# Kernel optimization log

Measured on AMD Instinct MI355X. Metric: run time of the kernel, lower is better.

The kernel has to match this reference:

```python
import jax, jax.numpy as jnp
import numpy as np

HSIZE, ESIZE, RSIZE = 256, 32, 64
STEP = 8  # dist=32, step=dist/4
B, A, T = 32, 128, 64

# 16 directional grid-cell bounds, shape [16,1,1] (matches torch constants)
_XMIN = jnp.array([STEP, 0, -STEP, -2 * STEP] * 4, jnp.float32).reshape(16, 1, 1)
_XMAX = jnp.array([2 * STEP, STEP, 0, -STEP] * 4, jnp.float32).reshape(16, 1, 1)
_YMIN = jnp.repeat(jnp.array([-2 * STEP, -STEP, 0, STEP], jnp.float32), 4).reshape(16, 1, 1)
_YMAX = jnp.repeat(jnp.array([-STEP, 0, STEP, 2 * STEP], jnp.float32), 4).reshape(16, 1, 1)


def setup_inputs() -> dict:
    key = jax.random.key(0)
    ks = jax.random.split(key, 20)
    w = lambda k, shape, s=0.05: jax.random.normal(k, shape, jnp.float32) * s
    data = jax.random.uniform(ks[0], (B, A, T, 2), jnp.float32) * 36.0 - 4.0
    return {
        "data": data,
        "tprob": 0,
        "W_r": w(ks[1], (RSIZE, 2)), "b_r": jnp.zeros((RSIZE,), jnp.float32),
        "W_e": w(ks[2], (ESIZE, HSIZE)), "b_e": jnp.zeros((ESIZE,), jnp.float32),
        "W_ih": w(ks[3], (4 * HSIZE, ESIZE * 16 + RSIZE)),
        "W_hh": w(ks[4], (4 * HSIZE, HSIZE)),
        "b_ih": jnp.zeros((4 * HSIZE,), jnp.float32),
        "b_hh": jnp.zeros((4 * HSIZE,), jnp.float32),
        "W_p": w(ks[5], (64, HSIZE + RSIZE)), "b_p": jnp.zeros((64,), jnp.float32),
        "W_p2": w(ks[6], (32, 64)), "b_p2": jnp.zeros((32,), jnp.float32),
        "W_mu": w(ks[7], (2, 32)), "b_mu": jnp.zeros((2,), jnp.float32),
        "W_sd": w(ks[8], (2, 32)), "b_sd": jnp.zeros((2,), jnp.float32),
        "W_cr": w(ks[9], (1, 32)), "b_cr": jnp.zeros((1,), jnp.float32),
    }


def _social(xy, h):
    # xy: [B,A,2] positions, h: [B,A,HSIZE] hidden states
    b, a = xy.shape[0], xy.shape[1]
    diff = xy[:, :, None, :] - xy[:, None, :, :]          # [B,A,A,2], (i,j)=x_i-x_j
    dx = diff[..., 0][:, None, :, :]                       # [B,1,A,A]
    dy = diff[..., 1][:, None, :, :]
    mask = (dx >= _XMIN) & (dx <= _XMAX) & (dy >= _YMIN) & (dy <= _YMAX)  # [B,16,A,A]
    active = xy[:, :, 0] >= 0                              # inactive: x<0
    mask = mask & active[:, None, :, None] & active[:, None, None, :]
    mask = mask & (~jnp.eye(a, dtype=bool))[None, None]    # zero diagonal
    # bmm: aggregate neighbor hiddens per grid cell
    return jnp.einsum('bgij,bjh->bgih', mask.astype(h.dtype), h)  # [B,16,A,HSIZE]


def reference(data, tprob, W_r, b_r, W_e, b_e, W_ih, W_hh, b_ih, b_hh,
              W_p, b_p, W_p2, b_p2, W_mu, b_mu, W_sd, b_sd, W_cr, b_cr):
    # tprob=0 -> teach_prob all zeros (no teacher forcing); dropout in eval mode.
    b, a, t, _ = data.shape
    h0 = jnp.zeros((b * a, HSIZE), data.dtype)
    c0 = jnp.zeros((b * a, HSIZE), data.dtype)

    def step(carry, xt):  # xt: [B,A,2]
        h, c = carry
        r = jax.nn.relu(xt @ W_r.T + b_r)                          # [B,A,64]
        Hs = _social(xt, h.reshape(b, a, HSIZE))                   # [B,16,A,256]
        e = jax.nn.relu(jnp.einsum('bgah,eh->bgae', Hs, W_e) + b_e)  # [B,16,A,32]
        e = e.reshape(b, a, 16 * ESIZE)                            # torch-style reshape
        inp = jnp.concatenate([r, e], -1).reshape(b * a, RSIZE + 16 * ESIZE)
        gates = inp @ W_ih.T + b_ih + h @ W_hh.T + b_hh
        ig, fg, gg, og = jnp.split(gates, 4, axis=-1)              # torch gate order i,f,g,o
        c2 = jax.nn.sigmoid(fg) * c + jax.nn.sigmoid(ig) * jnp.tanh(gg)
        h2 = jax.nn.sigmoid(og) * jnp.tanh(c2)
        inp2 = jnp.concatenate([r, h2.reshape(b, a, HSIZE)], -1)   # [B,A,320]
        out = (inp2 @ W_p.T + b_p) @ W_p2.T + b_p2                 # no activation (as in source)
        mu = out @ W_mu.T + b_mu
        sd = jnp.exp(out @ W_sd.T + b_sd)
        cr = jnp.tanh(out @ W_cr.T + b_cr)
        return (h2, c2), (mu, sd, cr)

    xs = jnp.moveaxis(data, 2, 0)                                  # [T,B,A,2]
    _, (mus, sds, crs) = jax.lax.scan(step, (h0, c0), xs)
    # stack along dim 2 -> [B,A,T,*]
    return (jnp.moveaxis(mus, 0, 2), jnp.moveaxis(sds, 0, 2), jnp.moveaxis(crs, 0, 2))
```

## Files before the change

### kernel.cpp

```cpp
#include <hip/hip_runtime.h>
#include <hip/hip_bf16.h>

#define B_  32
#define A_  128
#define T_  64
#define N_  4096
#define HS  256
#define ES  32
#define RS  64
#define KX  832
#define GD  1024
#define NKT 26

typedef __attribute__((ext_vector_type(8))) short bf8_t;
typedef __attribute__((ext_vector_type(8))) unsigned short u16x8;
typedef __attribute__((ext_vector_type(4))) float f4_t;
typedef __attribute__((ext_vector_type(2))) float f2_t;

__device__ __forceinline__ unsigned short f2bf(float x) {
  union { float f; unsigned u; } v; v.f = x;
  unsigned u = v.u;
  u += 0x7fffu + ((u >> 16) & 1u);
  return (unsigned short)(u >> 16);
}
__device__ __forceinline__ float bf2f(unsigned short u) {
  union { unsigned u; float f; } v; v.u = ((unsigned)u) << 16; return v.f;
}
__device__ __forceinline__ float sigm(float x) { return 1.f / (1.f + __expf(-x)); }

__device__ __forceinline__ void gload16(const void* g, void* l) {
  __builtin_amdgcn_global_load_lds((const __attribute__((address_space(1))) void*)g,
                                   (__attribute__((address_space(3))) void*)l, 16, 0, 0);
}

__global__ void k_wcat(const float* __restrict__ W_ih, const float* __restrict__ W_hh,
                       const float* __restrict__ b_ih, const float* __restrict__ b_hh,
                       const float* __restrict__ W_e,
                       unsigned short* __restrict__ Wc, float* __restrict__ bsum,
                       unsigned short* __restrict__ Web) {
  int i = blockIdx.x * 256 + threadIdx.x;
  if (i < GD * KX) {
    int mp = i / KX, k = i - mp * KX;
    int nb = mp >> 6, rem = mp & 63, g = rem >> 4, q = rem & 15;
    int mo = g * 256 + nb * 16 + q;
    float v = (k < 576) ? W_ih[mo * 576 + k] : W_hh[mo * 256 + (k - 576)];
    Wc[i] = f2bf(v);
  } else if (i < GD * KX + GD) {
    int j = i - GD * KX;
    int nb = j >> 6, rem = j & 63, g = rem >> 4, q = rem & 15;
    int mo = g * 256 + nb * 16 + q;
    bsum[j] = b_ih[mo] + b_hh[mo];
  } else if (i < GD * KX + GD + ES * HS) {
    int j2 = i - GD * KX - GD;
    Web[j2] = f2bf(W_e[j2]);
  }
}

__global__ __launch_bounds__(320) void k_head(
    const float* __restrict__ W_p, const float* __restrict__ b_p,
    const float* __restrict__ W_p2, const float* __restrict__ b_p2,
    const float* __restrict__ W_mu, const float* __restrict__ b_mu,
    const float* __restrict__ W_sd, const float* __restrict__ b_sd,
    const float* __restrict__ W_cr, const float* __restrict__ b_cr,
    float* __restrict__ Whead, float* __restrict__ bhead) {
  int o = blockIdx.x, tid = threadIdx.x;
  __shared__ float to[64];
  const float* Wo = (o < 2) ? W_mu + o * 32 : (o < 4) ? W_sd + (o - 2) * 32 : W_cr;
  if (tid < 64) {
    float a = 0.f;
    #pragma unroll 8
    for (int c = 0; c < 32; ++c) a += Wo[c] * W_p2[c * 64 + tid];
    to[tid] = a;
  }
  __syncthreads();
  float a = 0.f;
  #pragma unroll 8
  for (int j = 0; j < 64; ++j) a += to[j] * W_p[j * 320 + tid];
  Whead[o * 320 + tid] = a;
  if (tid == 0) {
    float b0 = (o < 2) ? b_mu[o] : (o < 4) ? b_sd[o - 2] : b_cr[0];
    float acc = b0;
    for (int c = 0; c < 32; ++c) acc += Wo[c] * b_p2[c];
    for (int j = 0; j < 64; ++j) acc += to[j] * b_p[j];
    bhead[o] = acc;
  }
}

__device__ __forceinline__ void head_fin_dev(
    const float* __restrict__ data, const float* __restrict__ W_r,
    const float* __restrict__ b_r, const float* __restrict__ Whead,
    const float* __restrict__ bhead, const unsigned short* __restrict__ Xh,
    float* __restrict__ out, int n0, int ts, int tid) {
  int r8 = tid >> 5, ln = tid & 31;
  int n = n0 + r8;
  float s0 = 0.f, s1 = 0.f, s2 = 0.f, s3 = 0.f, s4 = 0.f;
  u16x8 hv = *(const u16x8*)(Xh + (size_t)n * KX + 576 + ln * 8);
  float hf[8];
  #pragma unroll
  for (int k = 0; k < 8; ++k) hf[k] = bf2f(hv[k]);
  #pragma unroll
  for (int k = 0; k < 8; ++k) {
    int kk = 64 + ln * 8 + k;
    s0 += hf[k] * Whead[0 * 320 + kk];
    s1 += hf[k] * Whead[1 * 320 + kk];
    s2 += hf[k] * Whead[2 * 320 + kk];
    s3 += hf[k] * Whead[3 * 320 + kk];
    s4 += hf[k] * Whead[4 * 320 + kk];
  }
  float x0 = data[(n * T_ + ts) * 2 + 0];
  float x1 = data[(n * T_ + ts) * 2 + 1];
  #pragma unroll
  for (int l2 = 0; l2 < 2; ++l2) {
    int l = ln + 32 * l2;
    float rv = fmaxf(x0 * W_r[l * 2] + x1 * W_r[l * 2 + 1] + b_r[l], 0.f);
    s0 += rv * Whead[0 * 320 + l];
    s1 += rv * Whead[1 * 320 + l];
    s2 += rv * Whead[2 * 320 + l];
    s3 += rv * Whead[3 * 320 + l];
    s4 += rv * Whead[4 * 320 + l];
  }
  #pragma unroll
  for (int off = 16; off; off >>= 1) {
    s0 += __shfl_xor(s0, off);
    s1 += __shfl_xor(s1, off);
    s2 += __shfl_xor(s2, off);
    s3 += __shfl_xor(s3, off);
    s4 += __shfl_xor(s4, off);
  }
  if (ln == 0) {
    out[(n * T_ + ts) * 2 + 0] = s0 + bhead[0];
    out[(n * T_ + ts) * 2 + 1] = s1 + bhead[1];
    out[N_ * T_ * 2 + (n * T_ + ts) * 2 + 0] = __expf(s2 + bhead[2]);
    out[N_ * T_ * 2 + (n * T_ + ts) * 2 + 1] = __expf(s3 + bhead[3]);
    out[N_ * T_ * 4 + n * T_ + ts] = tanhf(s4 + bhead[4]);
  }
}

__global__ __launch_bounds__(256) void k_social(
    const float* __restrict__ data, const unsigned short* __restrict__ Web,
    const float* __restrict__ b_e, unsigned short* __restrict__ Xcur,
    const float* __restrict__ Whead, const float* __restrict__ bhead,
    const float* __restrict__ W_r, const float* __restrict__ b_r,
    float* __restrict__ out, int t) {
  int b  = blockIdx.x >> 4;
  int ig = blockIdx.x & 15;
  int n0 = b * A_ + ig * 8;
  __shared__ float sx[A_], sy[A_];
  __shared__ float shw2[64 * 64];
  __shared__ float smx[8][64][8];
  __shared__ float smy[8][64][8];
  int tid = threadIdx.x;
  if (tid < A_) {
    sx[tid] = data[((b * A_ + tid) * T_ + t) * 2 + 0];
    sy[tid] = data[((b * A_ + tid) * T_ + t) * 2 + 1];
  }
  if (t > 0)
    head_fin_dev(data, W_r, b_r, Whead, bhead, Xcur, out, n0, t - 1, tid);
  for (int u = tid; u < 512; u += 256) {
    int rr = u >> 6, l = u & 63;
    int n = n0 + rr;
    float x0 = data[(n * T_ + t) * 2 + 0];
    float x1 = data[(n * T_ + t) * 2 + 1];
    Xcur[(size_t)n * KX + l] =
        f2bf(fmaxf(x0 * W_r[l * 2] + x1 * W_r[l * 2 + 1] + b_r[l], 0.f));
  }
  {
    int wv = tid >> 6, lane = tid & 63;
    int lr = lane & 15, lh = lane >> 4;
    const unsigned short* a0p = Xcur + (size_t)(b * A_ + wv * 32 + lr) * KX + 576 + lh * 8;
    const unsigned short* a1p = a0p + 16 * KX;
    const unsigned short* b0p = Web + lr * HS + lh * 8;
    const unsigned short* b1p = Web + (16 + lr) * HS + lh * 8;
    f4_t hacc[2][2];
    hacc[0][0] = (f4_t){0.f,0.f,0.f,0.f}; hacc[0][1] = hacc[0][0];
    hacc[1][0] = hacc[0][0];              hacc[1][1] = hacc[0][0];
    #pragma unroll
    for (int kk = 0; kk < 8; ++kk) {
      bf8_t av0 = *(const bf8_t*)(a0p + kk * 32);
      bf8_t av1 = *(const bf8_t*)(a1p + kk * 32);
      bf8_t bv0 = *(const bf8_t*)(b0p + kk * 32);
      bf8_t bv1 = *(const bf8_t*)(b1p + kk * 32);
      hacc[0][0] = __builtin_amdgcn_mfma_f32_16x16x32_bf16(av0, bv0, hacc[0][0], 0, 0, 0);
      hacc[0][1] = __builtin_amdgcn_mfma_f32_16x16x32_bf16(av0, bv1, hacc[0][1], 0, 0, 0);
      hacc[1][0] = __builtin_amdgcn_mfma_f32_16x16x32_bf16(av1, bv0, hacc[1][0], 0, 0, 0);
      hacc[1][1] = __builtin_amdgcn_mfma_f32_16x16x32_bf16(av1, bv1, hacc[1][1], 0, 0, 0);
    }
    int ccol = lane & 15, crow4 = (lane >> 4) * 4;
    #pragma unroll
    for (int m = 0; m < 2; ++m)
      #pragma unroll
      for (int cb2 = 0; cb2 < 2; ++cb2)
        #pragma unroll
        for (int j = 0; j < 4; ++j) {
          int rr = wv * 32 + m * 16 + crow4 + j;
          int c  = cb2 * 16 + ccol;
          shw2[(rr >> 1) * 64 + c * 2 + (rr & 1)] = hacc[m][cb2][j];
        }
  }
  __syncthreads();

  for (int u = tid; u < 512; u += 256) {
    int r = u >> 6, jp = u & 63;
    int irow = ig * 8 + r;
    float xi = sx[irow], yi = sy[irow];
    bool acti = xi >= 0.f;
    float m0[4], m1[4], nn0[4], nn1[4];
    #pragma unroll
    for (int s = 0; s < 2; ++s) {
      int j = jp * 2 + s;
      float xj = sx[j], yj = sy[j];
      bool v = acti && (xj >= 0.f) && (j != irow);
      float dx = xi - xj, dy = yi - yj;
      float* mm = s ? m1 : m0;
      float* nn = s ? nn1 : nn0;
      mm[0] = (v && dx >= 8.f   && dx <= 16.f) ? 1.f : 0.f;
      mm[1] = (v && dx >= 0.f   && dx <= 8.f ) ? 1.f : 0.f;
      mm[2] = (v && dx >= -8.f  && dx <= 0.f ) ? 1.f : 0.f;
      mm[3] = (v && dx >= -16.f && dx <= -8.f) ? 1.f : 0.f;
      nn[0] = (dy >= -16.f && dy <= -8.f) ? 1.f : 0.f;
      nn[1] = (dy >= -8.f  && dy <= 0.f ) ? 1.f : 0.f;
      nn[2] = (dy >= 0.f   && dy <= 8.f ) ? 1.f : 0.f;
      nn[3] = (dy >= 8.f   && dy <= 16.f) ? 1.f : 0.f;
    }
    float4* px = (float4*)&smx[r][jp][0];
    px[0] = (float4){m0[0], m1[0], m0[1], m1[1]};
    px[1] = (float4){m0[2], m1[2], m0[3], m1[3]};
    float4* py = (float4*)&smy[r][jp][0];
    py[0] = (float4){nn0[0], nn1[0], nn0[1], nn1[1]};
    py[1] = (float4){nn0[2], nn1[2], nn0[3], nn1[3]};
  }
  __syncthreads();

  int half = tid >> 5;
  int lane = tid & 31;
  f2_t acc[16];
  #pragma unroll
  for (int g = 0; g < 16; ++g) acc[g] = (f2_t){0.f, 0.f};
  #pragma unroll 2
  for (int jp = 0; jp < 64; ++jp) {
    f2_t hv = *(const f2_t*)&shw2[jp * 64 + lane * 2];
    float4 xa = ((const float4*)&smx[half][jp][0])[0];
    float4 xb = ((const float4*)&smx[half][jp][0])[1];
    float4 ya = ((const float4*)&smy[half][jp][0])[0];
    float4 yb = ((const float4*)&smy[half][jp][0])[1];
    f2_t mx[4] = {(f2_t){xa.x, xa.y}, (f2_t){xa.z, xa.w},
                  (f2_t){xb.x, xb.y}, (f2_t){xb.z, xb.w}};
    f2_t p[4]  = {(f2_t){ya.x, ya.y} * hv, (f2_t){ya.z, ya.w} * hv,
                  (f2_t){yb.x, yb.y} * hv, (f2_t){yb.z, yb.w} * hv};
    #pragma unroll
    for (int gy = 0; gy < 4; ++gy)
      #pragma unroll
      for (int gx = 0; gx < 4; ++gx)
        acc[gy * 4 + gx] += mx[gx] * p[gy];
  }

  int irow = ig * 8 + half;
  float be = b_e[lane];
  int hi = irow >> 4;
  int klo = (irow & 15) * ES + lane;
  #pragma unroll
  for (int g = 0; g < 16; ++g) {
    float e = fmaxf(acc[g][0] + acc[g][1] + be, 0.f);
    int a_out = g * 8 + hi;
    Xcur[(b * A_ + a_out) * KX + 64 + klo] = f2bf(e);
  }
}

__global__ __launch_bounds__(512) void k_gemm_lstm(
    const unsigned short* __restrict__ Xcur, const unsigned short* __restrict__ Wc,
    const float* __restrict__ bsum,
    float* __restrict__ cbuf, unsigned short* __restrict__ Xnext) {
  __shared__ unsigned short sA0[128 * 32];
  __shared__ unsigned short sB0[128 * 32];
  __shared__ unsigned short sA1[128 * 32];
  __shared__ unsigned short sB1[128 * 32];

  int bid = blockIdx.x;
  int tm = bid & 31, tc = bid >> 5;
  int row0 = tm * 128, col0 = tc * 128;
  int tid = threadIdx.x;
  int lane = tid & 63;
  int w = tid >> 6;
  int wr = w >> 1, wc = w & 1;
  int lr = lane & 15, lh = lane >> 4;

  int srow = tid >> 2, schunk = tid & 3;
  int gch = (schunk ^ ((srow >> 1) & 3)) * 8;
  const unsigned short* gA = Xcur + (size_t)(row0 + srow) * KX + gch;
  const unsigned short* gB = Wc  + (size_t)(col0 + srow) * KX + gch;

  int swz = (lh ^ ((lr >> 1) & 3)) * 8;
  int aoff[2], boff[4];
  #pragma unroll
  for (int m = 0; m < 2; ++m) aoff[m] = (wr * 32 + m * 16 + lr) * 32 + swz;
  #pragma unroll
  for (int n = 0; n < 4; ++n) boff[n] = (wc * 64 + n * 16 + lr) * 32 + swz;

  int q = lane & 15;
  float bias_g[4];
  #pragma unroll
  for (int n = 0; n < 4; ++n) bias_g[n] = bsum[col0 + wc * 64 + n * 16 + q];

  f4_t acc[2][4];
  #pragma unroll
  for (int m = 0; m < 2; ++m)
    #pragma unroll
    for (int n = 0; n < 4; ++n) acc[m][n] = (f4_t){0.f, 0.f, 0.f, 0.f};

#define STAGE(pA, pB, kt) do { \
    gload16(gA + (kt) * 32, (pA) + tid * 8); \
    gload16(gB + (kt) * 32, (pB) + tid * 8); \
  } while (0)

#define COMPUTE(pA, pB) do { \
    bf8_t a_[2], b_[4]; \
    _Pragma("unroll") for (int m = 0; m < 2; ++m) a_[m] = *(const bf8_t*)((pA) + aoff[m]); \
    _Pragma("unroll") for (int n = 0; n < 4; ++n) b_[n] = *(const bf8_t*)((pB) + boff[n]); \
    _Pragma("unroll") for (int m = 0; m < 2; ++m) \
      _Pragma("unroll") for (int n = 0; n < 4; ++n) \
        acc[m][n] = __builtin_amdgcn_mfma_f32_16x16x32_bf16(a_[m], b_[n], acc[m][n], 0, 0, 0); \
  } while (0)

  STAGE(sA0, sB0, 0);
  __syncthreads();
  #pragma unroll 1
  for (int kt = 0; kt < NKT; kt += 2) {
    STAGE(sA1, sB1, kt + 1);
    COMPUTE(sA0, sB0);
    __syncthreads();
    if (kt + 2 < NKT) STAGE(sA0, sB0, kt + 2);
    COMPUTE(sA1, sB1);
    __syncthreads();
  }
#undef STAGE
#undef COMPUTE

  int ch = (tc * 2 + wc) * 16 + q;
  int jrow4 = (lane >> 4) * 4;
  #pragma unroll
  for (int m = 0; m < 2; ++m) {
    #pragma unroll
    for (int j = 0; j < 4; ++j) {
      int row = row0 + wr * 32 + m * 16 + jrow4 + j;
      float ig = acc[m][0][j] + bias_g[0];
      float fg = acc[m][1][j] + bias_g[1];
      float gg = acc[m][2][j] + bias_g[2];
      float og = acc[m][3][j] + bias_g[3];
      float cold = cbuf[(size_t)row * HS + ch];
      float c2 = sigm(fg) * cold + sigm(ig) * tanhf(gg);
      float h2 = sigm(og) * tanhf(c2);
      cbuf[(size_t)row * HS + ch] = c2;
      Xnext[(size_t)row * KX + 576 + ch] = f2bf(h2);
    }
  }
}

__global__ __launch_bounds__(256) void k_fin(
    const float* __restrict__ data, const float* __restrict__ W_r,
    const float* __restrict__ b_r, const float* __restrict__ Whead,
    const float* __restrict__ bhead, const unsigned short* __restrict__ Xh,
    float* __restrict__ out) {
  head_fin_dev(data, W_r, b_r, Whead, bhead, Xh, out,
               blockIdx.x * 8, T_ - 1, threadIdx.x);
}

extern "C" void kernel_launch(void* const* d_in, const int* in_sizes, int n_in,
                              void* d_out, int out_size, void* d_ws, size_t ws_size,
                              hipStream_t stream) {
  const float* data = (const float*)d_in[0];
  const float* W_r  = (const float*)d_in[2];
  const float* b_r  = (const float*)d_in[3];
  const float* W_e  = (const float*)d_in[4];
  const float* b_e  = (const float*)d_in[5];
  const float* W_ih = (const float*)d_in[6];
  const float* W_hh = (const float*)d_in[7];
  const float* b_ih = (const float*)d_in[8];
  const float* b_hh = (const float*)d_in[9];
  const float* W_p  = (const float*)d_in[10];
  const float* b_p  = (const float*)d_in[11];
  const float* W_p2 = (const float*)d_in[12];
  const float* b_p2 = (const float*)d_in[13];
  const float* W_mu = (const float*)d_in[14];
  const float* b_mu = (const float*)d_in[15];
  const float* W_sd = (const float*)d_in[16];
  const float* b_sd = (const float*)d_in[17];
  const float* W_cr = (const float*)d_in[18];
  const float* b_cr = (const float*)d_in[19];
  float* out = (float*)d_out;

  char* ws = (char*)d_ws;
  float* cbuf  = (float*)(ws);
  unsigned short* Xbf0 = (unsigned short*)(ws + (4u  << 20));
  unsigned short* Xbf1 = (unsigned short*)(ws + (11u << 20));
  unsigned short* Wc   = (unsigned short*)(ws + (18u << 20));
  float* bsum  = (float*)(ws + (20u << 20));
  float* Whead = (float*)(ws + (20u << 20) + 8192);
  float* bhead = (float*)(ws + (20u << 20) + 16384);
  unsigned short* Web = (unsigned short*)(ws + (20u << 20) + 20480);

  hipMemsetAsync(cbuf, 0, (size_t)N_ * HS * sizeof(float), stream);
  hipMemsetAsync(Xbf0, 0, (size_t)N_ * KX * sizeof(unsigned short), stream);

  k_wcat<<<(GD * KX + GD + ES * HS + 255) / 256, 256, 0, stream>>>(
      W_ih, W_hh, b_ih, b_hh, W_e, Wc, bsum, Web);
  k_head<<<5, 320, 0, stream>>>(W_p, b_p, W_p2, b_p2, W_mu, b_mu, W_sd, b_sd, W_cr, b_cr,
                                Whead, bhead);

  for (int t = 0; t < T_; ++t) {
    unsigned short* Xcur  = (t & 1) ? Xbf1 : Xbf0;
    unsigned short* Xnext = (t & 1) ? Xbf0 : Xbf1;
    k_social<<<512, 256, 0, stream>>>(data, Web, b_e, Xcur, Whead, bhead,
                                      W_r, b_r, out, t);
    k_gemm_lstm<<<256, 512, 0, stream>>>(Xcur, Wc, bsum, cbuf, Xnext);
  }
  k_fin<<<512, 256, 0, stream>>>(data, W_r, b_r, Whead, bhead, Xbf0, out);
}
```

Baseline: 2.378 ms.

## Enlarge social blocks, double GEMM K-tile, and special-case first timestep

Each social block now handles 16 agents with 512 threads, so the per-batch hidden-to-embedding MFMA is recomputed half as often. The LSTM GEMM stages 64-wide K tiles with an 8-way swizzle, which halves the number of barrier rounds. The t==0 step skips the embedding GEMM, zeroes its own h slots and ignores the old cell state, which lets the two workspace memsets be dropped. Risks: larger shared memory use lowers occupancy, the loop counts are hardcoded to K=832, and correctness depends on t==0 zeroing every h slot that later reads touch.

```diff
diff --git a/kernel.cpp b/kernel.cpp
--- a/kernel.cpp
+++ b/kernel.cpp
@@ -10,7 +10,6 @@
 #define RS  64
 #define KX  832
 #define GD  1024
-#define NKT 26
 
 typedef __attribute__((ext_vector_type(8))) short bf8_t;
 typedef __attribute__((ext_vector_type(8))) unsigned short u16x8;
@@ -136,19 +135,19 @@
   }
 }
 
-__global__ __launch_bounds__(256) void k_social(
+__global__ __launch_bounds__(512) void k_social(
     const float* __restrict__ data, const unsigned short* __restrict__ Web,
     const float* __restrict__ b_e, unsigned short* __restrict__ Xcur,
     const float* __restrict__ Whead, const float* __restrict__ bhead,
     const float* __restrict__ W_r, const float* __restrict__ b_r,
     float* __restrict__ out, int t) {
-  int b  = blockIdx.x >> 4;
-  int ig = blockIdx.x & 15;
-  int n0 = b * A_ + ig * 8;
+  int b   = blockIdx.x >> 3;
+  int ig8 = blockIdx.x & 7;
+  int n0  = b * A_ + ig8 * 16;
   __shared__ float sx[A_], sy[A_];
   __shared__ float shw2[64 * 64];
-  __shared__ float smx[8][64][8];
-  __shared__ float smy[8][64][8];
+  __shared__ float smx[16][64][8];
+  __shared__ float smy[16][64][8];
   int tid = threadIdx.x;
   if (tid < A_) {
     sx[tid] = data[((b * A_ + tid) * T_ + t) * 2 + 0];
@@ -156,7 +155,7 @@
   }
   if (t > 0)
     head_fin_dev(data, W_r, b_r, Whead, bhead, Xcur, out, n0, t - 1, tid);
-  for (int u = tid; u < 512; u += 256) {
+  for (int u = tid; u < 1024; u += 512) {
     int rr = u >> 6, l = u & 63;
     int n = n0 + rr;
     float x0 = data[(n * T_ + t) * 2 + 0];
@@ -164,44 +163,42 @@
     Xcur[(size_t)n * KX + l] =
         f2bf(fmaxf(x0 * W_r[l * 2] + x1 * W_r[l * 2 + 1] + b_r[l], 0.f));
   }
-  {
-    int wv = tid >> 6, lane = tid & 63;
+  if (t == 0) {
+    for (int i = tid; i < 64 * 64; i += 512) shw2[i] = 0.f;
+    u16x8 z = (u16x8){0, 0, 0, 0, 0, 0, 0, 0};
+    int row = tid >> 5, c8 = tid & 31;
+    *(u16x8*)(Xcur + (size_t)(n0 + row) * KX + 576 + c8 * 8) = z;
+  } else {
+    int w = tid >> 6, lane = tid & 63;
     int lr = lane & 15, lh = lane >> 4;
-    const unsigned short* a0p = Xcur + (size_t)(b * A_ + wv * 32 + lr) * KX + 576 + lh * 8;
-    const unsigned short* a1p = a0p + 16 * KX;
+    const unsigned short* a0p = Xcur + (size_t)(b * A_ + w * 16 + lr) * KX + 576 + lh * 8;
     const unsigned short* b0p = Web + lr * HS + lh * 8;
     const unsigned short* b1p = Web + (16 + lr) * HS + lh * 8;
-    f4_t hacc[2][2];
-    hacc[0][0] = (f4_t){0.f,0.f,0.f,0.f}; hacc[0][1] = hacc[0][0];
-    hacc[1][0] = hacc[0][0];              hacc[1][1] = hacc[0][0];
+    f4_t hacc[2];
+    hacc[0] = (f4_t){0.f, 0.f, 0.f, 0.f}; hacc[1] = hacc[0];
     #pragma unroll
     for (int kk = 0; kk < 8; ++kk) {
-      bf8_t av0 = *(const bf8_t*)(a0p + kk * 32);
-      bf8_t av1 = *(const bf8_t*)(a1p + kk * 32);
+      bf8_t av  = *(const bf8_t*)(a0p + kk * 32);
       bf8_t bv0 = *(const bf8_t*)(b0p + kk * 32);
       bf8_t bv1 = *(const bf8_t*)(b1p + kk * 32);
-      hacc[0][0] = __builtin_amdgcn_mfma_f32_16x16x32_bf16(av0, bv0, hacc[0][0], 0, 0, 0);
-      hacc[0][1] = __builtin_amdgcn_mfma_f32_16x16x32_bf16(av0, bv1, hacc[0][1], 0, 0, 0);
-      hacc[1][0] = __builtin_amdgcn_mfma_f32_16x16x32_bf16(av1, bv0, hacc[1][0], 0, 0, 0);
-      hacc[1][1] = __builtin_amdgcn_mfma_f32_16x16x32_bf16(av1, bv1, hacc[1][1], 0, 0, 0);
+      hacc[0] = __builtin_amdgcn_mfma_f32_16x16x32_bf16(av, bv0, hacc[0], 0, 0, 0);
+      hacc[1] = __builtin_amdgcn_mfma_f32_16x16x32_bf16(av, bv1, hacc[1], 0, 0, 0);
     }
     int ccol = lane & 15, crow4 = (lane >> 4) * 4;
     #pragma unroll
-    for (int m = 0; m < 2; ++m)
+    for (int cb2 = 0; cb2 < 2; ++cb2)
       #pragma unroll
-      for (int cb2 = 0; cb2 < 2; ++cb2)
-        #pragma unroll
-        for (int j = 0; j < 4; ++j) {
-          int rr = wv * 32 + m * 16 + crow4 + j;
-          int c  = cb2 * 16 + ccol;
-          shw2[(rr >> 1) * 64 + c * 2 + (rr & 1)] = hacc[m][cb2][j];
-        }
+      for (int j = 0; j < 4; ++j) {
+        int rr = w * 16 + crow4 + j;
+        int c  = cb2 * 16 + ccol;
+        shw2[(rr >> 1) * 64 + c * 2 + (rr & 1)] = hacc[cb2][j];
+      }
   }
   __syncthreads();
 
-  for (int u = tid; u < 512; u += 256) {
+  for (int u = tid; u < 1024; u += 512) {
     int r = u >> 6, jp = u & 63;
-    int irow = ig * 8 + r;
+    int irow = ig8 * 16 + r;
     float xi = sx[irow], yi = sy[irow];
     bool acti = xi >= 0.f;
     float m0[4], m1[4], nn0[4], nn1[4];
@@ -254,7 +251,7 @@
         acc[gy * 4 + gx] += mx[gx] * p[gy];
   }
 
-  int irow = ig * 8 + half;
+  int irow = ig8 * 16 + half;
   float be = b_e[lane];
   int hi = irow >> 4;
   int klo = (irow & 15) * ES + lane;
@@ -262,18 +259,18 @@
   for (int g = 0; g < 16; ++g) {
     float e = fmaxf(acc[g][0] + acc[g][1] + be, 0.f);
     int a_out = g * 8 + hi;
-    Xcur[(b * A_ + a_out) * KX + 64 + klo] = f2bf(e);
+    Xcur[(size_t)(b * A_ + a_out) * KX + 64 + klo] = f2bf(e);
   }
 }
 
 __global__ __launch_bounds__(512) void k_gemm_lstm(
     const unsigned short* __restrict__ Xcur, const unsigned short* __restrict__ Wc,
     const float* __restrict__ bsum,
-    float* __restrict__ cbuf, unsigned short* __restrict__ Xnext) {
-  __shared__ unsigned short sA0[128 * 32];
-  __shared__ unsigned short sB0[128 * 32];
-  __shared__ unsigned short sA1[128 * 32];
-  __shared__ unsigned short sB1[128 * 32];
+    float* __restrict__ cbuf, unsigned short* __restrict__ Xnext, int t) {
+  __shared__ unsigned short sA0[128 * 64];
+  __shared__ unsigned short sB0[128 * 64];
+  __shared__ unsigned short sA1[128 * 64];
+  __shared__ unsigned short sB1[128 * 64];
 
   int bid = blockIdx.x;
   int tm = bid & 31, tc = bid >> 5;
@@ -284,17 +281,22 @@
   int wr = w >> 1, wc = w & 1;
   int lr = lane & 15, lh = lane >> 4;
 
-  int srow = tid >> 2, schunk = tid & 3;
-  int gch = (schunk ^ ((srow >> 1) & 3)) * 8;
+  int srow = tid >> 3, schunk = tid & 7;
+  int gch = (schunk ^ ((srow >> 1) & 7)) * 8;
   const unsigned short* gA = Xcur + (size_t)(row0 + srow) * KX + gch;
   const unsigned short* gB = Wc  + (size_t)(col0 + srow) * KX + gch;
 
-  int swz = (lh ^ ((lr >> 1) & 3)) * 8;
-  int aoff[2], boff[4];
-  #pragma unroll
-  for (int m = 0; m < 2; ++m) aoff[m] = (wr * 32 + m * 16 + lr) * 32 + swz;
-  #pragma unroll
-  for (int n = 0; n < 4; ++n) boff[n] = (wc * 64 + n * 16 + lr) * 32 + swz;
+  int aoff[2][2], boff[4][2];
+  #pragma unroll
+  for (int m = 0; m < 2; ++m)
+    #pragma unroll
+    for (int kk = 0; kk < 2; ++kk)
+      aoff[m][kk] = (wr * 32 + m * 16 + lr) * 64 + ((kk * 4 + lh) ^ ((lr >> 1) & 7)) * 8;
+  #pragma unroll
+  for (int n = 0; n < 4; ++n)
+    #pragma unroll
+    for (int kk = 0; kk < 2; ++kk)
+      boff[n][kk] = (wc * 64 + n * 16 + lr) * 64 + ((kk * 4 + lh) ^ ((lr >> 1) & 7)) * 8;
 
   int q = lane & 15;
   float bias_g[4];
@@ -308,30 +310,35 @@
     for (int n = 0; n < 4; ++n) acc[m][n] = (f4_t){0.f, 0.f, 0.f, 0.f};
 
 #define STAGE(pA, pB, kt) do { \
-    gload16(gA + (kt) * 32, (pA) + tid * 8); \
-    gload16(gB + (kt) * 32, (pB) + tid * 8); \
+    gload16(gA + (size_t)(kt) * 64, (pA) + tid * 8); \
+    gload16(gA + (size_t)64 * KX + (kt) * 64, (pA) + 4096 + tid * 8); \
+    gload16(gB + (size_t)(kt) * 64, (pB) + tid * 8); \
+    gload16(gB + (size_t)64 * KX + (kt) * 64, (pB) + 4096 + tid * 8); \
   } while (0)
 
 #define COMPUTE(pA, pB) do { \
-    bf8_t a_[2], b_[4]; \
-    _Pragma("unroll") for (int m = 0; m < 2; ++m) a_[m] = *(const bf8_t*)((pA) + aoff[m]); \
-    _Pragma("unroll") for (int n = 0; n < 4; ++n) b_[n] = *(const bf8_t*)((pB) + boff[n]); \
-    _Pragma("unroll") for (int m = 0; m < 2; ++m) \
-      _Pragma("unroll") for (int n = 0; n < 4; ++n) \
-        acc[m][n] = __builtin_amdgcn_mfma_f32_16x16x32_bf16(a_[m], b_[n], acc[m][n], 0, 0, 0); \
+    _Pragma("unroll") for (int kk = 0; kk < 2; ++kk) { \
+      bf8_t a_[2], b_[4]; \
+      _Pragma("unroll") for (int m = 0; m < 2; ++m) a_[m] = *(const bf8_t*)((pA) + aoff[m][kk]); \
+      _Pragma("unroll") for (int n = 0; n < 4; ++n) b_[n] = *(const bf8_t*)((pB) + boff[n][kk]); \
+      _Pragma("unroll") for (int m = 0; m < 2; ++m) \
+        _Pragma("unroll") for (int n = 0; n < 4; ++n) \
+          acc[m][n] = __builtin_amdgcn_mfma_f32_16x16x32_bf16(a_[m], b_[n], acc[m][n], 0, 0, 0); \
+    } \
   } while (0)
 
   STAGE(sA0, sB0, 0);
   __syncthreads();
   #pragma unroll 1
-  for (int kt = 0; kt < NKT; kt += 2) {
+  for (int kt = 0; kt < 12; kt += 2) {
     STAGE(sA1, sB1, kt + 1);
     COMPUTE(sA0, sB0);
     __syncthreads();
-    if (kt + 2 < NKT) STAGE(sA0, sB0, kt + 2);
+    STAGE(sA0, sB0, kt + 2);
     COMPUTE(sA1, sB1);
     __syncthreads();
   }
+  COMPUTE(sA0, sB0);
 #undef STAGE
 #undef COMPUTE
 
@@ -346,7 +353,7 @@
       float fg = acc[m][1][j] + bias_g[1];
       float gg = acc[m][2][j] + bias_g[2];
       float og = acc[m][3][j] + bias_g[3];
-      float cold = cbuf[(size_t)row * HS + ch];
+      float cold = (t == 0) ? 0.f : cbuf[(size_t)row * HS + ch];
       float c2 = sigm(fg) * cold + sigm(ig) * tanhf(gg);
       float h2 = sigm(og) * tanhf(c2);
       cbuf[(size_t)row * HS + ch] = c2;
@@ -398,9 +405,6 @@
   float* bhead = (float*)(ws + (20u << 20) + 16384);
   unsigned short* Web = (unsigned short*)(ws + (20u << 20) + 20480);
 
-  hipMemsetAsync(cbuf, 0, (size_t)N_ * HS * sizeof(float), stream);
-  hipMemsetAsync(Xbf0, 0, (size_t)N_ * KX * sizeof(unsigned short), stream);
-
   k_wcat<<<(GD * KX + GD + ES * HS + 255) / 256, 256, 0, stream>>>(
       W_ih, W_hh, b_ih, b_hh, W_e, Wc, bsum, Web);
   k_head<<<5, 320, 0, stream>>>(W_p, b_p, W_p2, b_p2, W_mu, b_mu, W_sd, b_sd, W_cr, b_cr,
@@ -409,9 +413,9 @@
   for (int t = 0; t < T_; ++t) {
     unsigned short* Xcur  = (t & 1) ? Xbf1 : Xbf0;
     unsigned short* Xnext = (t & 1) ? Xbf0 : Xbf1;
-    k_social<<<512, 256, 0, stream>>>(data, Web, b_e, Xcur, Whead, bhead,
+    k_social<<<256, 512, 0, stream>>>(data, Web, b_e, Xcur, Whead, bhead,
                                       W_r, b_r, out, t);
-    k_gemm_lstm<<<256, 512, 0, stream>>>(Xcur, Wc, bsum, cbuf, Xnext);
+    k_gemm_lstm<<<256, 512, 0, stream>>>(Xcur, Wc, bsum, cbuf, Xnext, t);
   }
   k_fin<<<512, 256, 0, stream>>>(data, W_r, b_r, Whead, bhead, Xbf0, out);
 }
```

Measured after the change: 2.185 ms. -8.1%, faster.
